# Optimization experiments

Hardware: AMD Instinct MI355X
Metric: run time of the kernel (lower is better)

The kernel has to match this reference:

```python
import jax, jax.numpy as jnp
import numpy as np

B, TE, TD, HE, HD = 4, 512, 256, 128, 256

def setup_inputs() -> dict:
    key = jax.random.key(0)
    k1, k2, k3, k4, k5 = jax.random.split(key, 5)
    return {
        "encoder_out_seq": jax.random.normal(k1, (B, TE, HE), dtype=jnp.float32),
        "decoder_out_seq": jax.random.normal(k2, (B, TD, HD), dtype=jnp.float32),
        "W_a": jax.random.normal(k3, (HE, HE), dtype=jnp.float32) * 0.05,
        "U_a": jax.random.normal(k4, (HD, HE), dtype=jnp.float32) * 0.05,
        "V_a": jax.random.normal(k5, (HE, 1), dtype=jnp.float32) * 0.05,
    }

def reference(encoder_out_seq, decoder_out_seq, W_a, U_a, V_a):
    # Bahdanau additive attention, fully parallel over decoder steps
    # (the original K.rnn scan has no true recurrence: each step is independent).
    Ws = jnp.einsum('bse,ef->bsf', encoder_out_seq, W_a)   # [B,Te,He]
    Uh = jnp.einsum('btd,df->btf', decoder_out_seq, U_a)   # [B,Td,He]
    # [B,Td,Te,He] additive score features
    feat = jnp.tanh(Ws[:, None, :, :] + Uh[:, :, None, :])
    e = jnp.einsum('btsf,f->bts', feat, V_a[:, 0])         # [B,Td,Te]
    e = jax.nn.softmax(e, axis=-1)                         # attention weights
    c = jnp.einsum('bts,bse->bte', e, encoder_out_seq)     # [B,Td,He] contexts
    return (c, e)
```

## Files before the change

### kernel.cpp

```cpp
#include <hip/hip_runtime.h>

#define Bn  4
#define TEn 512
#define TDn 256
#define HEn 128
#define HDn 256

#define LOG2E 1.4426950408889634f
#define K2    2.8853900817779268f

__global__ __launch_bounds__(512) void prep_kernel(
    const float* __restrict__ enc, const float* __restrict__ W,
    const float* __restrict__ dec, const float* __restrict__ U,
    float* __restrict__ Ws, float* __restrict__ Uh)
{
    __shared__ __align__(16) float lds[2048];
    const int tid = threadIdx.x;
    if (blockIdx.x < 256) {
        const int r0 = blockIdx.x * 8;
        *(float2*)&lds[2 * tid] = *(const float2*)(enc + r0 * HEn + 2 * tid);
        __syncthreads();
        const int c2 = (tid & 63) * 2;
        const int rl = tid >> 6;
        const float* er = lds + rl * HEn;
        float a0 = 0.f, a1 = 0.f;
        #pragma unroll 4
        for (int k = 0; k < HEn; k += 4) {
            const float4 e4 = *(const float4*)(er + k);
            const float2 w0 = *(const float2*)(W + (k + 0) * HEn + c2);
            const float2 w1 = *(const float2*)(W + (k + 1) * HEn + c2);
            const float2 w2 = *(const float2*)(W + (k + 2) * HEn + c2);
            const float2 w3 = *(const float2*)(W + (k + 3) * HEn + c2);
            a0 = fmaf(e4.x, w0.x, a0); a1 = fmaf(e4.x, w0.y, a1);
            a0 = fmaf(e4.y, w1.x, a0); a1 = fmaf(e4.y, w1.y, a1);
            a0 = fmaf(e4.z, w2.x, a0); a1 = fmaf(e4.z, w2.y, a1);
            a0 = fmaf(e4.w, w3.x, a0); a1 = fmaf(e4.w, w3.y, a1);
        }
        float2 o; o.x = a0 * K2; o.y = a1 * K2;
        *(float2*)(Ws + (r0 + rl) * HEn + c2) = o;
    } else {
        const int r0 = (blockIdx.x - 256) * 4;
        *(float2*)&lds[2 * tid] = *(const float2*)(dec + r0 * HDn + 2 * tid);
        __syncthreads();
        const int f2 = (tid & 63) * 2;
        const int rl = (tid >> 6) & 3;
        const int kp = tid >> 8;
        const float* d = lds + rl * HDn + kp * 128;
        float a0 = 0.f, a1 = 0.f;
        #pragma unroll 4
        for (int k = 0; k < 128; k += 4) {
            const float4 d4 = *(const float4*)(d + k);
            const float2 u0 = *(const float2*)(U + (kp * 128 + k + 0) * HEn + f2);
            const float2 u1 = *(const float2*)(U + (kp * 128 + k + 1) * HEn + f2);
            const float2 u2 = *(const float2*)(U + (kp * 128 + k + 2) * HEn + f2);
            const float2 u3 = *(const float2*)(U + (kp * 128 + k + 3) * HEn + f2);
            a0 = fmaf(d4.x, u0.x, a0); a1 = fmaf(d4.x, u0.y, a1);
            a0 = fmaf(d4.y, u1.x, a0); a1 = fmaf(d4.y, u1.y, a1);
            a0 = fmaf(d4.z, u2.x, a0); a1 = fmaf(d4.z, u2.y, a1);
            a0 = fmaf(d4.w, u3.x, a0); a1 = fmaf(d4.w, u3.y, a1);
        }
        __syncthreads();
        __shared__ float part[2][4][HEn];
        part[kp][rl][f2]     = a0;
        part[kp][rl][f2 + 1] = a1;
        __syncthreads();
        if (kp == 0) {
            float2 o;
            o.x = (part[0][rl][f2]     + part[1][rl][f2])     * K2;
            o.y = (part[0][rl][f2 + 1] + part[1][rl][f2 + 1]) * K2;
            *(float2*)(Uh + (r0 + rl) * HEn + f2) = o;
        }
    }
}

__global__ __launch_bounds__(512, 4) void attn_fused_kernel(
    const float* __restrict__ enc, const float* __restrict__ V,
    const float* __restrict__ Ws, const float* __restrict__ Uh,
    float* __restrict__ c_out, float* __restrict__ e_out)
{
    const int bp   = blockIdx.x;
    const int b    = bp >> 7;
    const int bt0  = b * TDn + (bp & 127) * 2;
    const int tid  = threadIdx.x;
    const int lane = tid & 63;
    const int wave = tid >> 6;

    __shared__ __align__(16) float sc0[TEn];
    __shared__ __align__(16) float sc1[TEn];
    __shared__ __align__(16) float part[16][2 * HEn];
    __shared__ float redm[2][8];
    __shared__ float reds[2][8];

    {
        const int s_sub = lane & 7;
        const int f0    = (lane >> 3) * 16;
        float4 mv[4], u0[4], u1[4];
        float sv = 0.f;
        #pragma unroll
        for (int j = 0; j < 4; ++j) {
            const float4 v = *(const float4*)(V + f0 + 4 * j);
            sv += v.x + v.y + v.z + v.w;
            mv[j].x = -2.f * v.x; mv[j].y = -2.f * v.y;
            mv[j].z = -2.f * v.z; mv[j].w = -2.f * v.w;
            u0[j] = *(const float4*)(Uh + bt0 * HEn + f0 + 4 * j);
            u1[j] = *(const float4*)(Uh + (bt0 + 1) * HEn + f0 + 4 * j);
        }
        const float* wsb = Ws + (b * TEn + wave * 64) * HEn;
        #pragma unroll 2
        for (int ci = 0; ci < 8; ++ci) {
            const float* wp = wsb + (ci * 8 + s_sub) * HEn + f0;
            float x0 = sv, x1 = sv;
            #pragma unroll
            for (int j = 0; j < 4; ++j) {
                const float4 w = ((const float4*)wp)[j];
                float r;
                r = __builtin_amdgcn_rcpf(__builtin_amdgcn_exp2f(w.x + u0[j].x) + 1.f);
                x0 = fmaf(mv[j].x, r, x0);
                r = __builtin_amdgcn_rcpf(__builtin_amdgcn_exp2f(w.x + u1[j].x) + 1.f);
                x1 = fmaf(mv[j].x, r, x1);
                r = __builtin_amdgcn_rcpf(__builtin_amdgcn_exp2f(w.y + u0[j].y) + 1.f);
                x0 = fmaf(mv[j].y, r, x0);
                r = __builtin_amdgcn_rcpf(__builtin_amdgcn_exp2f(w.y + u1[j].y) + 1.f);
                x1 = fmaf(mv[j].y, r, x1);
                r = __builtin_amdgcn_rcpf(__builtin_amdgcn_exp2f(w.z + u0[j].z) + 1.f);
                x0 = fmaf(mv[j].z, r, x0);
                r = __builtin_amdgcn_rcpf(__builtin_amdgcn_exp2f(w.z + u1[j].z) + 1.f);
                x1 = fmaf(mv[j].z, r, x1);
                r = __builtin_amdgcn_rcpf(__builtin_amdgcn_exp2f(w.w + u0[j].w) + 1.f);
                x0 = fmaf(mv[j].w, r, x0);
                r = __builtin_amdgcn_rcpf(__builtin_amdgcn_exp2f(w.w + u1[j].w) + 1.f);
                x1 = fmaf(mv[j].w, r, x1);
            }
            x0 += __shfl_xor(x0, 8, 64);
            x1 += __shfl_xor(x1, 8, 64);
            x0 += __shfl_xor(x0, 16, 64);
            x1 += __shfl_xor(x1, 16, 64);
            x0 += __shfl_xor(x0, 32, 64);
            x1 += __shfl_xor(x1, 32, 64);
            if (lane < 8) {
                sc0[wave * 64 + ci * 8 + lane] = x0;
                sc1[wave * 64 + ci * 8 + lane] = x1;
            }
        }
    }
    __syncthreads();

    {
        const float v0 = sc0[tid];
        const float v1 = sc1[tid];
        float m0 = v0, m1 = v1;
        #pragma unroll
        for (int off = 32; off; off >>= 1) {
            m0 = fmaxf(m0, __shfl_xor(m0, off, 64));
            m1 = fmaxf(m1, __shfl_xor(m1, off, 64));
        }
        if (lane == 0) { redm[0][wave] = m0; redm[1][wave] = m1; }
        __syncthreads();
        float bm0 = redm[0][0], bm1 = redm[1][0];
        #pragma unroll
        for (int w = 1; w < 8; ++w) {
            bm0 = fmaxf(bm0, redm[0][w]);
            bm1 = fmaxf(bm1, redm[1][w]);
        }
        const float ex0 = __builtin_amdgcn_exp2f((v0 - bm0) * LOG2E);
        const float ex1 = __builtin_amdgcn_exp2f((v1 - bm1) * LOG2E);
        float s0 = ex0, s1 = ex1;
        #pragma unroll
        for (int off = 32; off; off >>= 1) {
            s0 += __shfl_xor(s0, off, 64);
            s1 += __shfl_xor(s1, off, 64);
        }
        if (lane == 0) { reds[0][wave] = s0; reds[1][wave] = s1; }
        __syncthreads();
        float bs0 = reds[0][0], bs1 = reds[1][0];
        #pragma unroll
        for (int w = 1; w < 8; ++w) { bs0 += reds[0][w]; bs1 += reds[1][w]; }
        const float e0 = ex0 * __builtin_amdgcn_rcpf(bs0);
        const float e1 = ex1 * __builtin_amdgcn_rcpf(bs1);
        e_out[bt0 * TEn + tid]       = e0;
        e_out[(bt0 + 1) * TEn + tid] = e1;
        sc0[tid] = e0;
        sc1[tid] = e1;
    }
    __syncthreads();

    {
        const int hl = tid & 31;
        const int sp = tid >> 5;
        const float* eb = enc + (b * TEn + sp * 32) * HEn + hl * 4;
        float4 a0 = {0,0,0,0}, a1 = {0,0,0,0};
        #pragma unroll 4
        for (int i = 0; i < 32; ++i) {
            const int s = sp * 32 + i;
            const float4 ev = *(const float4*)(eb + i * HEn);
            const float w0 = sc0[s], w1 = sc1[s];
            a0.x = fmaf(w0, ev.x, a0.x); a1.x = fmaf(w1, ev.x, a1.x);
            a0.y = fmaf(w0, ev.y, a0.y); a1.y = fmaf(w1, ev.y, a1.y);
            a0.z = fmaf(w0, ev.z, a0.z); a1.z = fmaf(w1, ev.z, a1.z);
            a0.w = fmaf(w0, ev.w, a0.w); a1.w = fmaf(w1, ev.w, a1.w);
        }
        *(float4*)&part[sp][hl * 4]       = a0;
        *(float4*)&part[sp][HEn + hl * 4] = a1;
    }
    __syncthreads();
    if (tid < 2 * HEn) {
        const int r = tid >> 7, h = tid & 127;
        float s = 0.f;
        #pragma unroll
        for (int p = 0; p < 16; ++p) s += part[p][r * HEn + h];
        c_out[(bt0 + r) * HEn + h] = s;
    }
}

extern "C" void kernel_launch(void* const* d_in, const int* in_sizes, int n_in,
                              void* d_out, int out_size, void* d_ws, size_t ws_size,
                              hipStream_t stream) {
    const float* enc = (const float*)d_in[0];
    const float* dec = (const float*)d_in[1];
    const float* W   = (const float*)d_in[2];
    const float* U   = (const float*)d_in[3];
    const float* V   = (const float*)d_in[4];
    float* out   = (float*)d_out;
    float* c_out = out;
    float* e_out = out + Bn * TDn * HEn;
    float* Ws    = (float*)d_ws;
    float* Uh    = (float*)d_ws + Bn * TEn * HEn;

    prep_kernel<<<512, 512, 0, stream>>>(enc, W, dec, U, Ws, Uh);
    attn_fused_kernel<<<Bn * TDn / 2, 512, 0, stream>>>(enc, V, Ws, Uh, c_out, e_out);
}
```

Measured before the change: 101.4 us.

## Fuse decoder projection Uh into attention kernel, shrink prep to Ws GEMM

The Uh = dec·U projection now runs inside each attention block: the block loads its two decoder rows into LDS, computes the two Uh rows with a 4-way K split and an LDS reduction, and keeps them in shared memory. The prep kernel now computes only Ws, using 256 blocks instead of 512. This drops the Uh workspace round trip and the prep work for Uh, but each attention block gains extra global reads of U (128 KB per block, mostly from cache), more shared memory, and two more barriers.

```diff
diff --git a/kernel.cpp b/kernel.cpp
--- a/kernel.cpp
+++ b/kernel.cpp
@@ -9,74 +9,40 @@
 #define LOG2E 1.4426950408889634f
 #define K2    2.8853900817779268f
 
-__global__ __launch_bounds__(512) void prep_kernel(
+__global__ __launch_bounds__(512) void ws_gemm_kernel(
     const float* __restrict__ enc, const float* __restrict__ W,
-    const float* __restrict__ dec, const float* __restrict__ U,
-    float* __restrict__ Ws, float* __restrict__ Uh)
+    float* __restrict__ Ws)
 {
-    __shared__ __align__(16) float lds[2048];
+    __shared__ __align__(16) float lds[8 * HEn];
     const int tid = threadIdx.x;
-    if (blockIdx.x < 256) {
-        const int r0 = blockIdx.x * 8;
-        *(float2*)&lds[2 * tid] = *(const float2*)(enc + r0 * HEn + 2 * tid);
-        __syncthreads();
-        const int c2 = (tid & 63) * 2;
-        const int rl = tid >> 6;
-        const float* er = lds + rl * HEn;
-        float a0 = 0.f, a1 = 0.f;
-        #pragma unroll 4
-        for (int k = 0; k < HEn; k += 4) {
-            const float4 e4 = *(const float4*)(er + k);
-            const float2 w0 = *(const float2*)(W + (k + 0) * HEn + c2);
-            const float2 w1 = *(const float2*)(W + (k + 1) * HEn + c2);
-            const float2 w2 = *(const float2*)(W + (k + 2) * HEn + c2);
-            const float2 w3 = *(const float2*)(W + (k + 3) * HEn + c2);
-            a0 = fmaf(e4.x, w0.x, a0); a1 = fmaf(e4.x, w0.y, a1);
-            a0 = fmaf(e4.y, w1.x, a0); a1 = fmaf(e4.y, w1.y, a1);
-            a0 = fmaf(e4.z, w2.x, a0); a1 = fmaf(e4.z, w2.y, a1);
-            a0 = fmaf(e4.w, w3.x, a0); a1 = fmaf(e4.w, w3.y, a1);
-        }
-        float2 o; o.x = a0 * K2; o.y = a1 * K2;
-        *(float2*)(Ws + (r0 + rl) * HEn + c2) = o;
-    } else {
-        const int r0 = (blockIdx.x - 256) * 4;
-        *(float2*)&lds[2 * tid] = *(const float2*)(dec + r0 * HDn + 2 * tid);
-        __syncthreads();
-        const int f2 = (tid & 63) * 2;
-        const int rl = (tid >> 6) & 3;
-        const int kp = tid >> 8;
-        const float* d = lds + rl * HDn + kp * 128;
-        float a0 = 0.f, a1 = 0.f;
-        #pragma unroll 4
-        for (int k = 0; k < 128; k += 4) {
-            const float4 d4 = *(const float4*)(d + k);
-            const float2 u0 = *(const float2*)(U + (kp * 128 + k + 0) * HEn + f2);
-            const float2 u1 = *(const float2*)(U + (kp * 128 + k + 1) * HEn + f2);
-            const float2 u2 = *(const float2*)(U + (kp * 128 + k + 2) * HEn + f2);
-            const float2 u3 = *(const float2*)(U + (kp * 128 + k + 3) * HEn + f2);
-            a0 = fmaf(d4.x, u0.x, a0); a1 = fmaf(d4.x, u0.y, a1);
-            a0 = fmaf(d4.y, u1.x, a0); a1 = fmaf(d4.y, u1.y, a1);
-            a0 = fmaf(d4.z, u2.x, a0); a1 = fmaf(d4.z, u2.y, a1);
-            a0 = fmaf(d4.w, u3.x, a0); a1 = fmaf(d4.w, u3.y, a1);
-        }
-        __syncthreads();
-        __shared__ float part[2][4][HEn];
-        part[kp][rl][f2]     = a0;
-        part[kp][rl][f2 + 1] = a1;
-        __syncthreads();
-        if (kp == 0) {
-            float2 o;
-            o.x = (part[0][rl][f2]     + part[1][rl][f2])     * K2;
-            o.y = (part[0][rl][f2 + 1] + part[1][rl][f2 + 1]) * K2;
-            *(float2*)(Uh + (r0 + rl) * HEn + f2) = o;
-        }
-    }
+    const int r0  = blockIdx.x * 8;
+    *(float2*)&lds[2 * tid] = *(const float2*)(enc + r0 * HEn + 2 * tid);
+    __syncthreads();
+    const int c2 = (tid & 63) * 2;
+    const int rl = tid >> 6;
+    const float* er = lds + rl * HEn;
+    float a0 = 0.f, a1 = 0.f;
+    #pragma unroll 4
+    for (int k = 0; k < HEn; k += 4) {
+        const float4 e4 = *(const float4*)(er + k);
+        const float2 w0 = *(const float2*)(W + (k + 0) * HEn + c2);
+        const float2 w1 = *(const float2*)(W + (k + 1) * HEn + c2);
+        const float2 w2 = *(const float2*)(W + (k + 2) * HEn + c2);
+        const float2 w3 = *(const float2*)(W + (k + 3) * HEn + c2);
+        a0 = fmaf(e4.x, w0.x, a0); a1 = fmaf(e4.x, w0.y, a1);
+        a0 = fmaf(e4.y, w1.x, a0); a1 = fmaf(e4.y, w1.y, a1);
+        a0 = fmaf(e4.z, w2.x, a0); a1 = fmaf(e4.z, w2.y, a1);
+        a0 = fmaf(e4.w, w3.x, a0); a1 = fmaf(e4.w, w3.y, a1);
+    }
+    float2 o; o.x = a0 * K2; o.y = a1 * K2;
+    *(float2*)(Ws + (r0 + rl) * HEn + c2) = o;
 }
 
-__global__ __launch_bounds__(512, 4) void attn_fused_kernel(
-    const float* __restrict__ enc, const float* __restrict__ V,
-    const float* __restrict__ Ws, const float* __restrict__ Uh,
-    float* __restrict__ c_out, float* __restrict__ e_out)
+__global__ __launch_bounds__(512, 4) void attn_kernel(
+    const float* __restrict__ enc, const float* __restrict__ dec,
+    const float* __restrict__ U, const float* __restrict__ V,
+    const float* __restrict__ Ws, float* __restrict__ c_out,
+    float* __restrict__ e_out)
 {
     const int bp   = blockIdx.x;
     const int b    = bp >> 7;
@@ -85,12 +51,43 @@
     const int lane = tid & 63;
     const int wave = tid >> 6;
 
+    __shared__ __align__(16) float dec_lds[2 * HDn];
+    __shared__ __align__(16) float uh0[HEn];
+    __shared__ __align__(16) float uh1[HEn];
     __shared__ __align__(16) float sc0[TEn];
     __shared__ __align__(16) float sc1[TEn];
     __shared__ __align__(16) float part[16][2 * HEn];
     __shared__ float redm[2][8];
     __shared__ float reds[2][8];
 
+    dec_lds[tid] = dec[bt0 * HDn + tid];
+    __syncthreads();
+
+    {
+        const int f = tid & 127;
+        const int p = tid >> 7;
+        const float* d0 = dec_lds + p * 64;
+        const float* d1 = dec_lds + HDn + p * 64;
+        const float* u  = U + (p * 64) * HEn + f;
+        float a0 = 0.f, a1 = 0.f;
+        #pragma unroll 8
+        for (int k = 0; k < 64; ++k) {
+            const float uk = u[k * HEn];
+            a0 = fmaf(d0[k], uk, a0);
+            a1 = fmaf(d1[k], uk, a1);
+        }
+        part[p][f]       = a0;
+        part[p][HEn + f] = a1;
+    }
+    __syncthreads();
+    if (tid < 2 * HEn) {
+        const int r = tid >> 7, f = tid & 127;
+        const float s = part[0][r * HEn + f] + part[1][r * HEn + f]
+                      + part[2][r * HEn + f] + part[3][r * HEn + f];
+        (r ? uh1 : uh0)[f] = s * K2;
+    }
+    __syncthreads();
+
     {
         const int s_sub = lane & 7;
         const int f0    = (lane >> 3) * 16;
@@ -102,8 +99,8 @@
             sv += v.x + v.y + v.z + v.w;
             mv[j].x = -2.f * v.x; mv[j].y = -2.f * v.y;
             mv[j].z = -2.f * v.z; mv[j].w = -2.f * v.w;
-            u0[j] = *(const float4*)(Uh + bt0 * HEn + f0 + 4 * j);
-            u1[j] = *(const float4*)(Uh + (bt0 + 1) * HEn + f0 + 4 * j);
+            u0[j] = *(const float4*)(uh0 + f0 + 4 * j);
+            u1[j] = *(const float4*)(uh1 + f0 + 4 * j);
         }
         const float* wsb = Ws + (b * TEn + wave * 64) * HEn;
         #pragma unroll 2
@@ -224,8 +221,7 @@
     float* c_out = out;
     float* e_out = out + Bn * TDn * HEn;
     float* Ws    = (float*)d_ws;
-    float* Uh    = (float*)d_ws + Bn * TEn * HEn;
-
-    prep_kernel<<<512, 512, 0, stream>>>(enc, W, dec, U, Ws, Uh);
-    attn_fused_kernel<<<Bn * TDn / 2, 512, 0, stream>>>(enc, V, Ws, Uh, c_out, e_out);
+
+    ws_gemm_kernel<<<Bn * TEn / 8, 512, 0, stream>>>(enc, W, Ws);
+    attn_kernel<<<Bn * TDn / 2, 512, 0, stream>>>(enc, dec, U, V, Ws, c_out, e_out);
 }
```

New measurement: 96.11 us. 1.05x faster.
